# Kernel optimization log

Measured on AMD Instinct MI355X. Metric: run time of the kernel, lower is better.

Reference implementation:

```python
import jax, jax.numpy as jnp
import numpy as np

N = 50000          # nodes
E = 800000         # edges (avg degree 16)
NODE_IN, NODE_OUT = 64, 96
EDGE_IN, EDGE_OUT = 32, 32
CONV = [192, 192]  # hidden_conv_sizes
LIN = [192]        # hidden_linear_sizes
NUM_CLASSES = 2


def _linear_init(k, fan_in, fan_out):
    s = 1.0 / np.sqrt(fan_in)
    kw, kb = jax.random.split(k)
    W = jax.random.uniform(kw, (fan_in, fan_out), jnp.float32, -s, s)
    b = jax.random.uniform(kb, (fan_out,), jnp.float32, -s, s)
    return W, b


def setup_inputs() -> dict:
    key = jax.random.key(0)
    ks = jax.random.split(key, 10)
    node_feats = jax.random.normal(ks[0], (N, NODE_IN), jnp.float32)
    edge_feats = jax.random.normal(ks[1], (E, EDGE_IN), jnp.float32)
    src = jax.random.randint(ks[2], (E,), 0, N)
    dst = jax.random.randint(ks[3], (E,), 0, N)
    Wn, bn = _linear_init(ks[4], NODE_IN, NODE_OUT)
    We, be = _linear_init(ks[5], EDGE_IN, EDGE_OUT)
    Wc0, bc0 = _linear_init(ks[6], NODE_OUT + EDGE_OUT, CONV[0])
    Wc1, bc1 = _linear_init(ks[7], CONV[0], CONV[1])
    Wl0, bl0 = _linear_init(ks[8], CONV[1], LIN[0])
    Wo, bo = _linear_init(ks[9], LIN[0], NUM_CLASSES)
    return dict(node_feats=node_feats, edge_feats=edge_feats,
                Wn=Wn, bn=bn, We=We, be=be,
                Wc0=Wc0, bc0=bc0, Wc1=Wc1, bc1=bc1,
                Wl0=Wl0, bl0=bl0, Wo=Wo, bo=bo,
                src=src, dst=dst)


def reference(node_feats, edge_feats, Wn, bn, We, be, Wc0, bc0, Wc1, bc1,
              Wl0, bl0, Wo, bo, src, dst):
    ones = jnp.ones((E,), jnp.float32)
    deg_in = jnp.clip(jax.ops.segment_sum(ones, dst, num_segments=N), 1.0)
    deg_out = jnp.clip(jax.ops.segment_sum(ones, src, num_segments=N), 1.0)
    inv_in = jax.lax.rsqrt(deg_in)    # D_in^{-1/2}
    inv_out = jax.lax.rsqrt(deg_out)  # D_out^{-1/2}

    # EdgeLayer: per-edge linear, mean-aggregated onto destination nodes
    eh = edge_feats @ We + be                                   # [E, EDGE_OUT]
    edge_h = jax.nn.relu(
        jax.ops.segment_sum(eh, dst, num_segments=N) / deg_in[:, None])

    # NodeEmbeddingLayer: per-node linear
    node_h = jax.nn.relu(node_feats @ Wn + bn)                  # [N, NODE_OUT]

    h = jnp.concatenate([edge_h, node_h], axis=1)               # [N, EDGE_OUT+NODE_OUT]

    # dgl GraphConv (norm='both'): D_in^{-1/2} A D_out^{-1/2} h W + b
    # dropout is identity in eval mode
    for W, b in ((Wc0, bc0), (Wc1, bc1)):
        msg = (h * inv_out[:, None])[src]                       # [E, d] gather
        agg = jax.ops.segment_sum(msg, dst, num_segments=N) * inv_in[:, None]
        h = jax.nn.relu(agg @ W + b)

    h = jax.nn.relu(h @ Wl0 + bl0)
    return h @ Wo + bo                                          # [N, NUM_CLASSES]
```

## Files before the change

kernel.cpp:

```cpp
#include <hip/hip_runtime.h>

#define NN 50000
#define NE 800000
#define CAP 64

#define NPB 128
#define NBKT 391
#define NBKT_PAD 512
#define BCAP 3072
#define CHUNK 4096

typedef unsigned short u16;
typedef unsigned int u32;
typedef unsigned long long u64;
typedef __attribute__((ext_vector_type(8))) short bf8_t;
typedef __attribute__((ext_vector_type(4))) float f4_t;

__device__ __forceinline__ u16 f2b(float f) {
    unsigned u = __float_as_uint(f);
    unsigned r = u + 0x7FFF + ((u >> 16) & 1);
    return (u16)(r >> 16);
}

__global__ __launch_bounds__(256) void partition_k(
    const int* __restrict__ src, const int* __restrict__ dst,
    int* __restrict__ deg_out, int* __restrict__ bktc,
    u64* __restrict__ part, int E) {
    __shared__ unsigned cnt[NBKT_PAD];
    __shared__ unsigned base[NBKT_PAD];
    __shared__ unsigned cur[NBKT_PAD];
    __shared__ unsigned gbase[NBKT_PAD];
    __shared__ unsigned wtot[4];
    __shared__ u64 staged[CHUNK];

    const int tid = threadIdx.x;
    const int lane = tid & 63;
    const int wid = tid >> 6;
    const int e0 = blockIdx.x * CHUNK;
    const int n = min(CHUNK, E - e0);

    for (int i = tid; i < NBKT_PAD; i += 256) cnt[i] = 0;
    __syncthreads();

    for (int i = tid; i < n; i += 256) {
        int d = dst[e0 + i];
        atomicAdd(&cnt[d >> 7], 1u);
    }
    __syncthreads();

    {
        unsigned a = cnt[2 * tid];
        unsigned b = cnt[2 * tid + 1];
        unsigned ps = a + b;
        unsigned inc = ps;
#pragma unroll
        for (int d = 1; d < 64; d <<= 1) {
            unsigned v = __shfl_up(inc, d);
            if (lane >= d) inc += v;
        }
        if (lane == 63) wtot[wid] = inc;
        __syncthreads();
        unsigned wb = 0;
#pragma unroll
        for (int k = 0; k < 4; ++k) wb += (k < wid) ? wtot[k] : 0;
        unsigned eb = wb + inc - ps;
        base[2 * tid] = eb;
        base[2 * tid + 1] = eb + a;
        cur[2 * tid] = eb;
        cur[2 * tid + 1] = eb + a;
    }
    __syncthreads();

    for (int i = tid; i < n; i += 256) {
        int e = e0 + i;
        int d = dst[e];
        int s = src[e];
        atomicAdd(deg_out + s, 1);
        unsigned p = atomicAdd(&cur[d >> 7], 1u);
        staged[p] = ((u64)(unsigned)e << 32) | (((u32)d << 16) | (u32)s);
    }
    __syncthreads();

    for (int b = tid; b < NBKT; b += 256) {
        unsigned c = cur[b] - base[b];
        if (c) gbase[b] = (unsigned)atomicAdd(&bktc[b], (int)c);
    }
    __syncthreads();

    for (int i = tid; i < n; i += 256) {
        u64 v = staged[i];
        int b = (int)((v >> 16) & 0xffffu) >> 7;
        unsigned idx = gbase[b] + ((unsigned)i - base[b]);
        if (idx < BCAP) part[(size_t)b * BCAP + idx] = v;
    }
}

__global__ __launch_bounds__(256) void fill_k(
    const u64* __restrict__ part, const int* __restrict__ bktc,
    int* __restrict__ csr_src, int* __restrict__ csr_eid,
    int* __restrict__ din, int n) {
    __shared__ unsigned cur[NPB];
    const int tid = threadIdx.x;
    const int b = blockIdx.x;
    const int node0 = b << 7;
    if (tid < NPB) cur[tid] = 0;
    __syncthreads();

    const int cnt = min(bktc[b], BCAP);
    const u64* p = part + (size_t)b * BCAP;
    for (int i = tid; i < cnt; i += 256) {
        u64 v = p[i];
        int s = (int)(v & 0xffffu);
        int d = (int)((v >> 16) & 0xffffu);
        int e = (int)(v >> 32);
        unsigned q = atomicAdd(&cur[d & (NPB - 1)], 1u);
        if (q < CAP) {
            csr_src[((size_t)d << 6) + q] = s;
            csr_eid[((size_t)d << 6) + q] = e;
        }
    }
    __syncthreads();
    if (tid < NPB) {
        int node = node0 + tid;
        if (node < n) {
            unsigned cq = min(cur[tid], (unsigned)CAP);
            din[node] = (int)cq;
            int end = (cq <= 32u) ? 32 : 64;
            for (int q = (int)cq; q < end; ++q)
                csr_eid[((size_t)node << 6) + q] = 0;
        }
    }
}

__global__ void make_inv_k(const int* __restrict__ deg_in, const int* __restrict__ deg_out,
                           float* __restrict__ inv_in, float* __restrict__ inv_out,
                           float* __restrict__ inv_mean, float* __restrict__ bcoef, int n) {
    int i = blockIdx.x * 256 + threadIdx.x;
    if (i < n) {
        int d_in = deg_in[i];
        float di = fmaxf((float)d_in, 1.0f);
        float dq = fmaxf((float)deg_out[i], 1.0f);
        inv_in[i]   = 1.0f / sqrtf(di);
        inv_out[i]  = 1.0f / sqrtf(dq);
        inv_mean[i] = 1.0f / di;
        bcoef[i]    = (d_in > 0) ? 1.0f : 0.0f;
    }
}

__global__ __launch_bounds__(256) void gather_e4_k(
    const float* __restrict__ ef, const int* __restrict__ csr_eid,
    const int* __restrict__ deg, float* __restrict__ efa) {
    const int lane = threadIdx.x & 63;
    const int node = __builtin_amdgcn_readfirstlane(blockIdx.x * 4 + (threadIdx.x >> 6));
    const int beg = node << 6;
    const int cnt = deg[node];
    const int g = lane >> 4;
    const int c = (lane & 15) * 2;

    float ax = 0.0f, ay = 0.0f;
    {
        int eidv[8];
#pragma unroll
        for (int j = 0; j < 8; ++j) eidv[j] = csr_eid[beg + 4 * j + g];
        float2 v[8];
#pragma unroll
        for (int j = 0; j < 8; ++j)
            v[j] = *(const float2*)(ef + (size_t)eidv[j] * 32 + c);
#pragma unroll
        for (int j = 0; j < 8; ++j)
            if (4 * j + g < cnt) { ax += v[j].x; ay += v[j].y; }
    }
    if (cnt > 32) {
        int eidv[8];
#pragma unroll
        for (int j = 0; j < 8; ++j) eidv[j] = csr_eid[beg + 32 + 4 * j + g];
        float2 v[8];
#pragma unroll
        for (int j = 0; j < 8; ++j)
            v[j] = *(const float2*)(ef + (size_t)eidv[j] * 32 + c);
#pragma unroll
        for (int j = 0; j < 8; ++j)
            if (32 + 4 * j + g < cnt) { ax += v[j].x; ay += v[j].y; }
    }
    ax += __shfl_down(ax, 16); ay += __shfl_down(ay, 16);
    ax += __shfl_down(ax, 32); ay += __shfl_down(ay, 32);
    if (lane < 16) {
        float2 o; o.x = ax; o.y = ay;
        *(float2*)(efa + (size_t)node * 32 + c) = o;
    }
}

template <int D, int LPT>
__global__ __launch_bounds__(256) void gather_b2_k(
    const u16* __restrict__ h, const int* __restrict__ csr,
    const int* __restrict__ deg, const float* __restrict__ inv_in,
    u16* __restrict__ agg) {
    constexpr int ACT = D / LPT;
    constexpr int NW = LPT / 2;
    const int lane = threadIdx.x & 63;
    const int node = __builtin_amdgcn_readfirstlane(blockIdx.x * 4 + (threadIdx.x >> 6));
    const int beg = node << 6;
    const int cnt = deg[node];
    const int off = (lane < ACT ? lane : ACT - 1) * LPT;

    float acc[LPT];
#pragma unroll
    for (int j = 0; j < LPT; ++j) acc[j] = 0.0f;

    const int nb = cnt >> 4;
    int idx[16];
    if (nb > 0) {
#pragma unroll
        for (int j = 0; j < 16; ++j) idx[j] = csr[beg + j];
    }
    for (int b = 0; b < nb; ++b) {
        unsigned lv[16][NW];
#pragma unroll
        for (int j = 0; j < 16; ++j) {
            const unsigned* p = (const unsigned*)(h + (size_t)idx[j] * D + off);
            if constexpr (NW == 2) {
                uint2 t = *(const uint2*)p;
                lv[j][0] = t.x; lv[j][1] = t.y;
            } else {
                lv[j][0] = *p;
            }
        }
        int nidx[16];
        const int nbase = beg + (b + 1) * 16;
        if (b + 1 < nb) {
#pragma unroll
            for (int j = 0; j < 16; ++j) nidx[j] = csr[nbase + j];
        }
#pragma unroll
        for (int j = 0; j < 16; ++j)
#pragma unroll
            for (int q = 0; q < NW; ++q) {
                unsigned u = lv[j][q];
                acc[2 * q]     += __uint_as_float(u << 16);
                acc[2 * q + 1] += __uint_as_float(u & 0xffff0000u);
            }
        if (b + 1 < nb) {
#pragma unroll
            for (int j = 0; j < 16; ++j) idx[j] = nidx[j];
        }
    }

    int tb = beg + (nb << 4);
    int rem = cnt & 15;
    if (rem >= 8) {
        int ti[8];
#pragma unroll
        for (int j = 0; j < 8; ++j) ti[j] = csr[tb + j];
        unsigned lv[8][NW];
#pragma unroll
        for (int j = 0; j < 8; ++j) {
            const unsigned* p = (const unsigned*)(h + (size_t)ti[j] * D + off);
            if constexpr (NW == 2) {
                uint2 t = *(const uint2*)p;
                lv[j][0] = t.x; lv[j][1] = t.y;
            } else {
                lv[j][0] = *p;
            }
        }
#pragma unroll
        for (int j = 0; j < 8; ++j)
#pragma unroll
            for (int q = 0; q < NW; ++q) {
                unsigned u = lv[j][q];
                acc[2 * q]     += __uint_as_float(u << 16);
                acc[2 * q + 1] += __uint_as_float(u & 0xffff0000u);
            }
        tb += 8;
        rem -= 8;
    }
    for (int t = 0; t < rem; ++t) {
        const unsigned* p = (const unsigned*)(h + (size_t)csr[tb + t] * D + off);
#pragma unroll
        for (int q = 0; q < NW; ++q) {
            unsigned u = p[q];
            acc[2 * q]     += __uint_as_float(u << 16);
            acc[2 * q + 1] += __uint_as_float(u & 0xffff0000u);
        }
    }

    if (lane < ACT) {
        float sc = inv_in[node];
        unsigned o[NW];
#pragma unroll
        for (int q = 0; q < NW; ++q)
            o[q] = (unsigned)f2b(acc[2 * q] * sc) | ((unsigned)f2b(acc[2 * q + 1] * sc) << 16);
        unsigned* dp = (unsigned*)(agg + (size_t)node * D + off);
        if constexpr (NW == 2) {
            uint2 t; t.x = o[0]; t.y = o[1];
            *(uint2*)dp = t;
        } else {
            *dp = o[0];
        }
    }
}

template <int D_IN, int D_OUT, bool SCALE, bool BROW>
__global__ __launch_bounds__(256) void gemm_tile_k(
    const float* __restrict__ in, int in_stride,
    const float* __restrict__ W, const float* __restrict__ bias,
    const float* __restrict__ scale, const float* __restrict__ brow,
    const float* __restrict__ posts,
    u16* __restrict__ out, int out_stride, int n) {
    constexpr int TMW = 8;
    constexpr int ROWS = TMW * 4;
    constexpr int NOUT = (D_OUT + 63) / 64;
    __shared__ float s_in[ROWS * D_IN];

    const int tid = threadIdx.x;
    const int lane = tid & 63;
    const int wave = tid >> 6;
    const int row0 = blockIdx.x * ROWS;

    constexpr int NV = ROWS * D_IN / 4;
    for (int i = tid; i < NV; i += 256) {
        int m = i / (D_IN / 4);
        int kv = i % (D_IN / 4);
        int row = min(row0 + m, n - 1);
        float4 v = *(const float4*)(in + (size_t)row * in_stride + kv * 4);
        if (SCALE) {
            float s = scale[row];
            v.x *= s; v.y *= s; v.z *= s; v.w *= s;
        }
        *(float4*)(s_in + m * D_IN + kv * 4) = v;
    }
    __syncthreads();

    int f[NOUT], ff[NOUT];
    bool fok[NOUT];
    float bv[NOUT];
#pragma unroll
    for (int o = 0; o < NOUT; ++o) {
        f[o] = lane + 64 * o;
        fok[o] = (f[o] < D_OUT);
        ff[o] = fok[o] ? f[o] : 0;
        bv[o] = bias[ff[o]];
    }

    const float* s_my = s_in + wave * TMW * D_IN;

    float acc[NOUT][TMW];
#pragma unroll
    for (int o = 0; o < NOUT; ++o)
#pragma unroll
        for (int m = 0; m < TMW; ++m) acc[o][m] = 0.0f;

    for (int k = 0; k < D_IN; k += 4) {
        float w[4][NOUT];
#pragma unroll
        for (int j = 0; j < 4; ++j)
#pragma unroll
            for (int o = 0; o < NOUT; ++o) w[j][o] = W[(k + j) * D_OUT + ff[o]];
#pragma unroll
        for (int m = 0; m < TMW; ++m) {
            float4 a = *(const float4*)(s_my + m * D_IN + k);
#pragma unroll
            for (int o = 0; o < NOUT; ++o) {
                acc[o][m] = fmaf(a.x, w[0][o], acc[o][m]);
                acc[o][m] = fmaf(a.y, w[1][o], acc[o][m]);
                acc[o][m] = fmaf(a.z, w[2][o], acc[o][m]);
                acc[o][m] = fmaf(a.w, w[3][o], acc[o][m]);
            }
        }
    }

#pragma unroll
    for (int m = 0; m < TMW; ++m) {
        int row = row0 + wave * TMW + m;
        if (row < n) {
            float bc = BROW ? brow[row] : 1.0f;
            float pm = posts[row];
#pragma unroll
            for (int o = 0; o < NOUT; ++o) {
                if (!fok[o]) continue;
                float v = fmaxf(acc[o][m] + bv[o] * bc, 0.0f) * pm;
                out[(size_t)row * out_stride + f[o]] = f2b(v);
            }
        }
    }
}

template <int K>
__global__ void pack_w_k(const float* __restrict__ W, u16* __restrict__ Wp) {
    constexpr int KS = K / 32;
    int idx = blockIdx.x * 256 + threadIdx.x;
    if (idx >= 12 * KS * 64) return;
    int l = idx & 63;
    int s = (idx >> 6) % KS;
    int t = (idx >> 6) / KS;
    int col = t * 16 + (l & 15);
    int krow = s * 32 + ((l >> 4) * 8);
    u16 tmp[8] __attribute__((aligned(16)));
#pragma unroll
    for (int j = 0; j < 8; ++j) tmp[j] = f2b(W[(size_t)(krow + j) * 192 + col]);
    *(uint4*)(Wp + (size_t)idx * 8) = *(const uint4*)tmp;
}

template <int K>
__global__ __launch_bounds__(256) void mfma_gemm_k(
    const u16* __restrict__ A, const u16* __restrict__ Wp,
    const float* __restrict__ bias, const float* __restrict__ posts,
    u16* __restrict__ outB, int n) {
    constexpr int KS = K / 32;
    const int tid = threadIdx.x;
    const int lane = tid & 63;
    const int w = tid >> 6;
    const int row0 = blockIdx.x * 16;
    const int arow = row0 + (lane & 15);
    const int kbase = (lane >> 4) * 8;

    f4_t acc[3];
#pragma unroll
    for (int o = 0; o < 3; ++o) acc[o] = (f4_t){0.f, 0.f, 0.f, 0.f};

    const u16* ap = A + (size_t)arow * K + kbase;
#pragma unroll
    for (int s = 0; s < KS; ++s) {
        bf8_t af = *(const bf8_t*)(ap + s * 32);
#pragma unroll
        for (int o = 0; o < 3; ++o) {
            int t = w * 3 + o;
            bf8_t bf = *(const bf8_t*)(Wp + (size_t)((t * KS + s) * 64 + lane) * 8);
            acc[o] = __builtin_amdgcn_mfma_f32_16x16x32_bf16(af, bf, acc[o], 0, 0, 0);
        }
    }

    const int drow = row0 + (lane >> 4) * 4;
    const int dcol = lane & 15;
    float pm[4];
#pragma unroll
    for (int r = 0; r < 4; ++r) pm[r] = posts[drow + r];
#pragma unroll
    for (int o = 0; o < 3; ++o) {
        int col = (w * 3 + o) * 16 + dcol;
        float bv = bias[col];
#pragma unroll
        for (int r = 0; r < 4; ++r) {
            float v = fmaxf(acc[o][r] + bv, 0.0f) * pm[r];
            outB[(size_t)(drow + r) * 192 + col] = f2b(v);
        }
    }
}

__global__ __launch_bounds__(256) void mfma_fused_k(
    const u16* __restrict__ A,
    const u16* __restrict__ Wp1, const float* __restrict__ b1,
    const u16* __restrict__ Wp2, const float* __restrict__ b2,
    const float* __restrict__ Wo, const float* __restrict__ bo,
    float* __restrict__ out, int n) {
    constexpr int KS = 6;
    constexpr int S = 200;
    __shared__ float sbuf[16 * S];
    __shared__ float s_head[16][17][2];

    const int tid = threadIdx.x;
    const int lane = tid & 63;
    const int w = tid >> 6;
    const int row0 = blockIdx.x * 16;
    const int arow = row0 + (lane & 15);
    const int kbase = (lane >> 4) * 8;
    const int drow = (lane >> 4) * 4;
    const int dcol = lane & 15;

    f4_t acc[3];
#pragma unroll
    for (int o = 0; o < 3; ++o) acc[o] = (f4_t){0.f, 0.f, 0.f, 0.f};

    const u16* ap = A + (size_t)arow * 192 + kbase;
#pragma unroll
    for (int s = 0; s < KS; ++s) {
        bf8_t af = *(const bf8_t*)(ap + s * 32);
#pragma unroll
        for (int o = 0; o < 3; ++o) {
            int t = w * 3 + o;
            bf8_t bf = *(const bf8_t*)(Wp1 + (size_t)((t * KS + s) * 64 + lane) * 8);
            acc[o] = __builtin_amdgcn_mfma_f32_16x16x32_bf16(af, bf, acc[o], 0, 0, 0);
        }
    }

    u16* h2 = (u16*)sbuf;
#pragma unroll
    for (int o = 0; o < 3; ++o) {
        int col = (w * 3 + o) * 16 + dcol;
        float bv = b1[col];
#pragma unroll
        for (int r = 0; r < 4; ++r)
            h2[(drow + r) * S + col] = f2b(fmaxf(acc[o][r] + bv, 0.0f));
    }
    __syncthreads();

#pragma unroll
    for (int o = 0; o < 3; ++o) acc[o] = (f4_t){0.f, 0.f, 0.f, 0.f};
    const u16* hp = h2 + (lane & 15) * S + kbase;
#pragma unroll
    for (int s = 0; s < KS; ++s) {
        bf8_t af = *(const bf8_t*)(hp + s * 32);
#pragma unroll
        for (int o = 0; o < 3; ++o) {
            int t = w * 3 + o;
            bf8_t bf = *(const bf8_t*)(Wp2 + (size_t)((t * KS + s) * 64 + lane) * 8);
            acc[o] = __builtin_amdgcn_mfma_f32_16x16x32_bf16(af, bf, acc[o], 0, 0, 0);
        }
    }
    __syncthreads();

#pragma unroll
    for (int o = 0; o < 3; ++o) {
        int col = (w * 3 + o) * 16 + dcol;
        float bv = b2[col];
#pragma unroll
        for (int r = 0; r < 4; ++r)
            sbuf[(drow + r) * S + col] = fmaxf(acc[o][r] + bv, 0.0f);
    }
    __syncthreads();

    {
        int r = tid >> 4;
        int seg = tid & 15;
        const float* hr = sbuf + r * S + seg * 12;
        const float* wor = Wo + seg * 24;
        float p0 = 0.0f, p1 = 0.0f;
#pragma unroll
        for (int c = 0; c < 12; ++c) {
            float hv = hr[c];
            p0 = fmaf(hv, wor[c * 2 + 0], p0);
            p1 = fmaf(hv, wor[c * 2 + 1], p1);
        }
        s_head[r][seg][0] = p0;
        s_head[r][seg][1] = p1;
    }
    __syncthreads();
    if (tid < 32) {
        int r = tid >> 1, c = tid & 1;
        float sum = bo[c];
#pragma unroll
        for (int g = 0; g < 16; ++g) sum += s_head[r][g][c];
        int row = row0 + r;
        if (row < n) out[(size_t)row * 2 + c] = sum;
    }
}

extern "C" void kernel_launch(void* const* d_in, const int* in_sizes, int n_in,
                              void* d_out, int out_size, void* d_ws, size_t ws_size,
                              hipStream_t stream) {
    const float* node_feats = (const float*)d_in[0];
    const float* edge_feats = (const float*)d_in[1];
    const float* Wn  = (const float*)d_in[2];
    const float* bn  = (const float*)d_in[3];
    const float* We  = (const float*)d_in[4];
    const float* be  = (const float*)d_in[5];
    const float* Wc0 = (const float*)d_in[6];
    const float* bc0 = (const float*)d_in[7];
    const float* Wc1 = (const float*)d_in[8];
    const float* bc1 = (const float*)d_in[9];
    const float* Wl0 = (const float*)d_in[10];
    const float* bl0 = (const float*)d_in[11];
    const float* Wo  = (const float*)d_in[12];
    const float* bo  = (const float*)d_in[13];
    const int* src = (const int*)d_in[14];
    const int* dst = (const int*)d_in[15];
    float* out = (float*)d_out;

    const int N = NN, E = NE;

    int* dout      = (int*)d_ws;
    int* bktc      = dout + N;
    int* din       = bktc + NBKT_PAD;
    int* csr_src   = din + N;
    int* csr_eid   = csr_src + (size_t)CAP * N;
    float* inv_in   = (float*)(csr_eid + (size_t)CAP * N);
    float* inv_out  = inv_in + N;
    float* inv_mean = inv_out + N;
    float* bcoef    = inv_mean + N;
    float* efa      = bcoef + N;
    u16* h0   = (u16*)(efa + (size_t)32 * N);
    u16* aggA = h0 + (size_t)128 * N;
    u16* h1   = aggA + (size_t)128 * N;
    u16* aggB = h1 + (size_t)192 * N;
    u16* Wp0  = aggB + (size_t)192 * N;
    u16* Wp1  = Wp0 + 128 * 192;
    u16* Wp2  = Wp1 + 192 * 192;
    u64* part = (u64*)h1;

    hipMemsetAsync(d_ws, 0, (size_t)(N + NBKT_PAD) * sizeof(int), stream);

    const int GB32 = (N + 31) / 32;
    const int GB16 = N / 16;
    const int GW4  = (N + 3) / 4;

    pack_w_k<128><<<dim3(12), dim3(256), 0, stream>>>(Wc0, Wp0);
    pack_w_k<192><<<dim3(18), dim3(256), 0, stream>>>(Wc1, Wp1);
    pack_w_k<192><<<dim3(18), dim3(256), 0, stream>>>(Wl0, Wp2);

    partition_k<<<dim3((E + CHUNK - 1) / CHUNK), dim3(256), 0, stream>>>(
        src, dst, dout, bktc, part, E);
    fill_k<<<dim3(NBKT), dim3(256), 0, stream>>>(part, bktc, csr_src, csr_eid, din, N);
    make_inv_k<<<dim3((N + 255) / 256), dim3(256), 0, stream>>>(din, dout, inv_in, inv_out,
                                                                inv_mean, bcoef, N);

    gather_e4_k<<<dim3(GW4), dim3(256), 0, stream>>>(edge_feats, csr_eid, din, efa);

    gemm_tile_k<32, 32, true, true><<<dim3(GB32), dim3(256), 0, stream>>>(
        efa, 32, We, be, inv_mean, bcoef, inv_out, h0, 128, N);
    gemm_tile_k<64, 96, false, false><<<dim3(GB32), dim3(256), 0, stream>>>(
        node_feats, 64, Wn, bn, nullptr, nullptr, inv_out, h0 + 32, 128, N);

    gather_b2_k<128, 2><<<dim3(GW4), dim3(256), 0, stream>>>(h0, csr_src, din, inv_in, aggA);
    mfma_gemm_k<128><<<dim3(GB16), dim3(256), 0, stream>>>(aggA, Wp0, bc0, inv_out, h1, N);

    gather_b2_k<192, 4><<<dim3(GW4), dim3(256), 0, stream>>>(h1, csr_src, din, inv_in, aggB);
    mfma_fused_k<<<dim3(GB16), dim3(256), 0, stream>>>(aggB, Wp1, bc1, Wp2, bl0, Wo, bo,
                                                       out, N);
}
```

Baseline: 429.6 us.

## Fuse weight packing, degree normalization, and edge/node embedding kernels

Weight packing is folded into extra blocks of the partition kernel, and the inverse-degree computation moves into fill_k. The edge gather, edge linear layer and node linear layer merge into one kernel, so the intermediate edge-aggregate buffer no longer goes through global memory. This cuts launches and memory traffic. In exchange, the edge linear is now computed per-wave with unsynchronized shared memory within a wave, and the node GEMM is specialized by hand.

```diff
diff --git a/kernel.cpp b/kernel.cpp
--- a/kernel.cpp
+++ b/kernel.cpp
@@ -9,6 +9,7 @@
 #define NBKT_PAD 512
 #define BCAP 3072
 #define CHUNK 4096
+#define GW4E 12500
 
 typedef unsigned short u16;
 typedef unsigned int u32;
@@ -22,10 +23,35 @@
     return (u16)(r >> 16);
 }
 
-__global__ __launch_bounds__(256) void partition_k(
+__device__ __forceinline__ void pack_one(const float* __restrict__ W, u16* __restrict__ Wp,
+                                         int idx, int KS) {
+    int l = idx & 63;
+    int s = (idx >> 6) % KS;
+    int t = (idx >> 6) / KS;
+    int col = t * 16 + (l & 15);
+    int krow = s * 32 + ((l >> 4) * 8);
+    u16 tmp[8] __attribute__((aligned(16)));
+#pragma unroll
+    for (int j = 0; j < 8; ++j) tmp[j] = f2b(W[(size_t)(krow + j) * 192 + col]);
+    *(uint4*)(Wp + (size_t)idx * 8) = *(const uint4*)tmp;
+}
+
+__global__ __launch_bounds__(256) void partition_pack_k(
     const int* __restrict__ src, const int* __restrict__ dst,
     int* __restrict__ deg_out, int* __restrict__ bktc,
-    u64* __restrict__ part, int E) {
+    u64* __restrict__ part, int E,
+    const float* __restrict__ Wc0, const float* __restrict__ Wc1,
+    const float* __restrict__ Wl0,
+    u16* __restrict__ Wp0, u16* __restrict__ Wp1, u16* __restrict__ Wp2) {
+    const int PBLK = (E + CHUNK - 1) / CHUNK;
+    if (blockIdx.x >= PBLK) {
+        int idx = (blockIdx.x - PBLK) * 256 + threadIdx.x;
+        if (idx < 3072) pack_one(Wc0, Wp0, idx, 4);
+        else if (idx < 7680) pack_one(Wc1, Wp1, idx - 3072, 6);
+        else if (idx < 12288) pack_one(Wl0, Wp2, idx - 7680, 6);
+        return;
+    }
+
     __shared__ unsigned cnt[NBKT_PAD];
     __shared__ unsigned base[NBKT_PAD];
     __shared__ unsigned cur[NBKT_PAD];
@@ -97,8 +123,11 @@
 
 __global__ __launch_bounds__(256) void fill_k(
     const u64* __restrict__ part, const int* __restrict__ bktc,
+    const int* __restrict__ deg_out,
     int* __restrict__ csr_src, int* __restrict__ csr_eid,
-    int* __restrict__ din, int n) {
+    int* __restrict__ din,
+    float* __restrict__ inv_in, float* __restrict__ inv_out,
+    float* __restrict__ inv_mean, float* __restrict__ bcoef, int n) {
     __shared__ unsigned cur[NPB];
     const int tid = threadIdx.x;
     const int b = blockIdx.x;
@@ -128,65 +157,135 @@
             int end = (cq <= 32u) ? 32 : 64;
             for (int q = (int)cq; q < end; ++q)
                 csr_eid[((size_t)node << 6) + q] = 0;
-        }
-    }
-}
-
-__global__ void make_inv_k(const int* __restrict__ deg_in, const int* __restrict__ deg_out,
-                           float* __restrict__ inv_in, float* __restrict__ inv_out,
-                           float* __restrict__ inv_mean, float* __restrict__ bcoef, int n) {
-    int i = blockIdx.x * 256 + threadIdx.x;
-    if (i < n) {
-        int d_in = deg_in[i];
-        float di = fmaxf((float)d_in, 1.0f);
-        float dq = fmaxf((float)deg_out[i], 1.0f);
-        inv_in[i]   = 1.0f / sqrtf(di);
-        inv_out[i]  = 1.0f / sqrtf(dq);
-        inv_mean[i] = 1.0f / di;
-        bcoef[i]    = (d_in > 0) ? 1.0f : 0.0f;
-    }
-}
-
-__global__ __launch_bounds__(256) void gather_e4_k(
+            float di = fmaxf((float)cq, 1.0f);
+            float dq = fmaxf((float)deg_out[node], 1.0f);
+            inv_in[node]   = 1.0f / sqrtf(di);
+            inv_out[node]  = 1.0f / sqrtf(dq);
+            inv_mean[node] = 1.0f / di;
+            bcoef[node]    = (cq > 0u) ? 1.0f : 0.0f;
+        }
+    }
+}
+
+__global__ __launch_bounds__(256) void edge_node_k(
     const float* __restrict__ ef, const int* __restrict__ csr_eid,
-    const int* __restrict__ deg, float* __restrict__ efa) {
-    const int lane = threadIdx.x & 63;
-    const int node = __builtin_amdgcn_readfirstlane(blockIdx.x * 4 + (threadIdx.x >> 6));
-    const int beg = node << 6;
-    const int cnt = deg[node];
-    const int g = lane >> 4;
-    const int c = (lane & 15) * 2;
-
-    float ax = 0.0f, ay = 0.0f;
-    {
-        int eidv[8];
-#pragma unroll
-        for (int j = 0; j < 8; ++j) eidv[j] = csr_eid[beg + 4 * j + g];
-        float2 v[8];
-#pragma unroll
-        for (int j = 0; j < 8; ++j)
-            v[j] = *(const float2*)(ef + (size_t)eidv[j] * 32 + c);
-#pragma unroll
-        for (int j = 0; j < 8; ++j)
-            if (4 * j + g < cnt) { ax += v[j].x; ay += v[j].y; }
-    }
-    if (cnt > 32) {
-        int eidv[8];
-#pragma unroll
-        for (int j = 0; j < 8; ++j) eidv[j] = csr_eid[beg + 32 + 4 * j + g];
-        float2 v[8];
-#pragma unroll
-        for (int j = 0; j < 8; ++j)
-            v[j] = *(const float2*)(ef + (size_t)eidv[j] * 32 + c);
-#pragma unroll
-        for (int j = 0; j < 8; ++j)
-            if (32 + 4 * j + g < cnt) { ax += v[j].x; ay += v[j].y; }
-    }
-    ax += __shfl_down(ax, 16); ay += __shfl_down(ay, 16);
-    ax += __shfl_down(ax, 32); ay += __shfl_down(ay, 32);
-    if (lane < 16) {
-        float2 o; o.x = ax; o.y = ay;
-        *(float2*)(efa + (size_t)node * 32 + c) = o;
+    const int* __restrict__ deg,
+    const float* __restrict__ inv_mean, const float* __restrict__ bcoef,
+    const float* __restrict__ inv_out,
+    const float* __restrict__ We, const float* __restrict__ be,
+    const float* __restrict__ nf, const float* __restrict__ Wn,
+    const float* __restrict__ bn,
+    u16* __restrict__ h0, int n) {
+    __shared__ float sv[4][32];
+    __shared__ float s_in[32 * 64];
+    const int tid = threadIdx.x;
+    const int lane = tid & 63;
+    const int w = tid >> 6;
+
+    if (blockIdx.x < GW4E) {
+        const int node = __builtin_amdgcn_readfirstlane(blockIdx.x * 4 + w);
+        const int beg = node << 6;
+        const int cnt = deg[node];
+        const int g = lane >> 4;
+        const int c = lane & 15;
+
+        float ax = 0.0f, ay = 0.0f;
+        {
+            int eidv[8];
+#pragma unroll
+            for (int j = 0; j < 8; ++j) eidv[j] = csr_eid[beg + 4 * j + g];
+            float2 v[8];
+#pragma unroll
+            for (int j = 0; j < 8; ++j)
+                v[j] = *(const float2*)(ef + (size_t)eidv[j] * 32 + 2 * c);
+#pragma unroll
+            for (int j = 0; j < 8; ++j)
+                if (4 * j + g < cnt) { ax += v[j].x; ay += v[j].y; }
+        }
+        if (cnt > 32) {
+            int eidv[8];
+#pragma unroll
+            for (int j = 0; j < 8; ++j) eidv[j] = csr_eid[beg + 32 + 4 * j + g];
+            float2 v[8];
+#pragma unroll
+            for (int j = 0; j < 8; ++j)
+                v[j] = *(const float2*)(ef + (size_t)eidv[j] * 32 + 2 * c);
+#pragma unroll
+            for (int j = 0; j < 8; ++j)
+                if (32 + 4 * j + g < cnt) { ax += v[j].x; ay += v[j].y; }
+        }
+        ax += __shfl_down(ax, 16); ay += __shfl_down(ay, 16);
+        ax += __shfl_down(ax, 32); ay += __shfl_down(ay, 32);
+        if (lane < 16) {
+            float im = inv_mean[node];
+            float2 o; o.x = ax * im; o.y = ay * im;
+            *(float2*)&sv[w][2 * c] = o;
+        }
+        int col = lane & 31;
+        float s = 0.0f;
+#pragma unroll 8
+        for (int k = 0; k < 32; ++k)
+            s = fmaf(sv[w][k], We[k * 32 + col], s);
+        if (lane < 32) {
+            float v = fmaxf(s + be[col] * bcoef[node], 0.0f) * inv_out[node];
+            h0[(size_t)node * 128 + col] = f2b(v);
+        }
+        return;
+    }
+
+    const int row0 = (blockIdx.x - GW4E) * 32;
+    for (int i = tid; i < 512; i += 256) {
+        int m = i >> 4;
+        int kv = i & 15;
+        int row = min(row0 + m, n - 1);
+        float4 v = *(const float4*)(nf + (size_t)row * 64 + kv * 4);
+        *(float4*)(s_in + m * 64 + kv * 4) = v;
+    }
+    __syncthreads();
+
+    int f0 = lane, f1 = lane + 64;
+    bool fok1 = (f1 < 96);
+    int ff1 = fok1 ? f1 : 0;
+    float bv0 = bn[f0], bv1 = bn[ff1];
+
+    const float* s_my = s_in + w * 8 * 64;
+    float acc0[8], acc1[8];
+#pragma unroll
+    for (int m = 0; m < 8; ++m) { acc0[m] = 0.0f; acc1[m] = 0.0f; }
+
+    for (int k = 0; k < 64; k += 4) {
+        float wv[4][2];
+#pragma unroll
+        for (int j = 0; j < 4; ++j) {
+            wv[j][0] = Wn[(k + j) * 96 + f0];
+            wv[j][1] = Wn[(k + j) * 96 + ff1];
+        }
+#pragma unroll
+        for (int m = 0; m < 8; ++m) {
+            float4 a = *(const float4*)(s_my + m * 64 + k);
+            acc0[m] = fmaf(a.x, wv[0][0], acc0[m]);
+            acc0[m] = fmaf(a.y, wv[1][0], acc0[m]);
+            acc0[m] = fmaf(a.z, wv[2][0], acc0[m]);
+            acc0[m] = fmaf(a.w, wv[3][0], acc0[m]);
+            acc1[m] = fmaf(a.x, wv[0][1], acc1[m]);
+            acc1[m] = fmaf(a.y, wv[1][1], acc1[m]);
+            acc1[m] = fmaf(a.z, wv[2][1], acc1[m]);
+            acc1[m] = fmaf(a.w, wv[3][1], acc1[m]);
+        }
+    }
+
+#pragma unroll
+    for (int m = 0; m < 8; ++m) {
+        int row = row0 + w * 8 + m;
+        if (row < n) {
+            float pm = inv_out[row];
+            float v0 = fmaxf(acc0[m] + bv0, 0.0f) * pm;
+            h0[(size_t)row * 128 + 32 + f0] = f2b(v0);
+            if (fok1) {
+                float v1 = fmaxf(acc1[m] + bv1, 0.0f) * pm;
+                h0[(size_t)row * 128 + 32 + f1] = f2b(v1);
+            }
+        }
     }
 }
 
@@ -297,107 +396,6 @@
             *dp = o[0];
         }
     }
-}
-
-template <int D_IN, int D_OUT, bool SCALE, bool BROW>
-__global__ __launch_bounds__(256) void gemm_tile_k(
-    const float* __restrict__ in, int in_stride,
-    const float* __restrict__ W, const float* __restrict__ bias,
-    const float* __restrict__ scale, const float* __restrict__ brow,
-    const float* __restrict__ posts,
-    u16* __restrict__ out, int out_stride, int n) {
-    constexpr int TMW = 8;
-    constexpr int ROWS = TMW * 4;
-    constexpr int NOUT = (D_OUT + 63) / 64;
-    __shared__ float s_in[ROWS * D_IN];
-
-    const int tid = threadIdx.x;
-    const int lane = tid & 63;
-    const int wave = tid >> 6;
-    const int row0 = blockIdx.x * ROWS;
-
-    constexpr int NV = ROWS * D_IN / 4;
-    for (int i = tid; i < NV; i += 256) {
-        int m = i / (D_IN / 4);
-        int kv = i % (D_IN / 4);
-        int row = min(row0 + m, n - 1);
-        float4 v = *(const float4*)(in + (size_t)row * in_stride + kv * 4);
-        if (SCALE) {
-            float s = scale[row];
-            v.x *= s; v.y *= s; v.z *= s; v.w *= s;
-        }
-        *(float4*)(s_in + m * D_IN + kv * 4) = v;
-    }
-    __syncthreads();
-
-    int f[NOUT], ff[NOUT];
-    bool fok[NOUT];
-    float bv[NOUT];
-#pragma unroll
-    for (int o = 0; o < NOUT; ++o) {
-        f[o] = lane + 64 * o;
-        fok[o] = (f[o] < D_OUT);
-        ff[o] = fok[o] ? f[o] : 0;
-        bv[o] = bias[ff[o]];
-    }
-
-    const float* s_my = s_in + wave * TMW * D_IN;
-
-    float acc[NOUT][TMW];
-#pragma unroll
-    for (int o = 0; o < NOUT; ++o)
-#pragma unroll
-        for (int m = 0; m < TMW; ++m) acc[o][m] = 0.0f;
-
-    for (int k = 0; k < D_IN; k += 4) {
-        float w[4][NOUT];
-#pragma unroll
-        for (int j = 0; j < 4; ++j)
-#pragma unroll
-            for (int o = 0; o < NOUT; ++o) w[j][o] = W[(k + j) * D_OUT + ff[o]];
-#pragma unroll
-        for (int m = 0; m < TMW; ++m) {
-            float4 a = *(const float4*)(s_my + m * D_IN + k);
-#pragma unroll
-            for (int o = 0; o < NOUT; ++o) {
-                acc[o][m] = fmaf(a.x, w[0][o], acc[o][m]);
-                acc[o][m] = fmaf(a.y, w[1][o], acc[o][m]);
-                acc[o][m] = fmaf(a.z, w[2][o], acc[o][m]);
-                acc[o][m] = fmaf(a.w, w[3][o], acc[o][m]);
-            }
-        }
-    }
-
-#pragma unroll
-    for (int m = 0; m < TMW; ++m) {
-        int row = row0 + wave * TMW + m;
-        if (row < n) {
-            float bc = BROW ? brow[row] : 1.0f;
-            float pm = posts[row];
-#pragma unroll
-            for (int o = 0; o < NOUT; ++o) {
-                if (!fok[o]) continue;
-                float v = fmaxf(acc[o][m] + bv[o] * bc, 0.0f) * pm;
-                out[(size_t)row * out_stride + f[o]] = f2b(v);
-            }
-        }
-    }
-}
-
-template <int K>
-__global__ void pack_w_k(const float* __restrict__ W, u16* __restrict__ Wp) {
-    constexpr int KS = K / 32;
-    int idx = blockIdx.x * 256 + threadIdx.x;
-    if (idx >= 12 * KS * 64) return;
-    int l = idx & 63;
-    int s = (idx >> 6) % KS;
-    int t = (idx >> 6) / KS;
-    int col = t * 16 + (l & 15);
-    int krow = s * 32 + ((l >> 4) * 8);
-    u16 tmp[8] __attribute__((aligned(16)));
-#pragma unroll
-    for (int j = 0; j < 8; ++j) tmp[j] = f2b(W[(size_t)(krow + j) * 192 + col]);
-    *(uint4*)(Wp + (size_t)idx * 8) = *(const uint4*)tmp;
 }
 
 template <int K>
@@ -576,8 +574,7 @@
     float* inv_out  = inv_in + N;
     float* inv_mean = inv_out + N;
     float* bcoef    = inv_mean + N;
-    float* efa      = bcoef + N;
-    u16* h0   = (u16*)(efa + (size_t)32 * N);
+    u16* h0   = (u16*)(bcoef + N);
     u16* aggA = h0 + (size_t)128 * N;
     u16* h1   = aggA + (size_t)128 * N;
     u16* aggB = h1 + (size_t)192 * N;
@@ -588,31 +585,23 @@
 
     hipMemsetAsync(d_ws, 0, (size_t)(N + NBKT_PAD) * sizeof(int), stream);
 
+    const int PBLK = (E + CHUNK - 1) / CHUNK;
+    const int GB16 = N / 16;
     const int GB32 = (N + 31) / 32;
-    const int GB16 = N / 16;
-    const int GW4  = (N + 3) / 4;
-
-    pack_w_k<128><<<dim3(12), dim3(256), 0, stream>>>(Wc0, Wp0);
-    pack_w_k<192><<<dim3(18), dim3(256), 0, stream>>>(Wc1, Wp1);
-    pack_w_k<192><<<dim3(18), dim3(256), 0, stream>>>(Wl0, Wp2);
-
-    partition_k<<<dim3((E + CHUNK - 1) / CHUNK), dim3(256), 0, stream>>>(
-        src, dst, dout, bktc, part, E);
-    fill_k<<<dim3(NBKT), dim3(256), 0, stream>>>(part, bktc, csr_src, csr_eid, din, N);
-    make_inv_k<<<dim3((N + 255) / 256), dim3(256), 0, stream>>>(din, dout, inv_in, inv_out,
-                                                                inv_mean, bcoef, N);
-
-    gather_e4_k<<<dim3(GW4), dim3(256), 0, stream>>>(edge_feats, csr_eid, din, efa);
-
-    gemm_tile_k<32, 32, true, true><<<dim3(GB32), dim3(256), 0, stream>>>(
-        efa, 32, We, be, inv_mean, bcoef, inv_out, h0, 128, N);
-    gemm_tile_k<64, 96, false, false><<<dim3(GB32), dim3(256), 0, stream>>>(
-        node_feats, 64, Wn, bn, nullptr, nullptr, inv_out, h0 + 32, 128, N);
-
-    gather_b2_k<128, 2><<<dim3(GW4), dim3(256), 0, stream>>>(h0, csr_src, din, inv_in, aggA);
+
+    partition_pack_k<<<dim3(PBLK + 48), dim3(256), 0, stream>>>(
+        src, dst, dout, bktc, part, E, Wc0, Wc1, Wl0, Wp0, Wp1, Wp2);
+    fill_k<<<dim3(NBKT), dim3(256), 0, stream>>>(part, bktc, dout, csr_src, csr_eid,
+                                                 din, inv_in, inv_out, inv_mean, bcoef, N);
+
+    edge_node_k<<<dim3(GW4E + GB32), dim3(256), 0, stream>>>(
+        edge_feats, csr_eid, din, inv_mean, bcoef, inv_out, We, be,
+        node_feats, Wn, bn, h0, N);
+
+    gather_b2_k<128, 2><<<dim3(GW4E), dim3(256), 0, stream>>>(h0, csr_src, din, inv_in, aggA);
     mfma_gemm_k<128><<<dim3(GB16), dim3(256), 0, stream>>>(aggA, Wp0, bc0, inv_out, h1, N);
 
-    gather_b2_k<192, 4><<<dim3(GW4), dim3(256), 0, stream>>>(h1, csr_src, din, inv_in, aggB);
+    gather_b2_k<192, 4><<<dim3(GW4E), dim3(256), 0, stream>>>(h1, csr_src, din, inv_in, aggB);
     mfma_fused_k<<<dim3(GB16), dim3(256), 0, stream>>>(aggB, Wp1, bc1, Wp2, bl0, Wo, bo,
                                                        out, N);
 }
```

Result: faster. 407.2 us (-5.2%).
